# Kernel tuning notes

Measured on AMD Instinct MI355X. Metric: run time of the kernel, lower is better.

The kernel has to match this reference:

```python
import jax, jax.numpy as jnp
import numpy as np

D = 4          # guide-feature dimension (in_channels_feature)
NV = D + 1     # simplex vertices / lattice remainders
BASE = 128     # per-coordinate key encoding base
OFF = 64
SENT = np.int32(2 ** 30)  # sentinel hash for unused slots


def _elevation_matrix(d):
    # Adams et al. elevation: cf = f * scale; elevated = E @ cf, built densely.
    E = np.zeros((d + 1, d), np.float32)
    E[0, :] = 1.0
    for i in range(1, d + 1):
        E[i, i - 1] = -i
        E[i, i:] = 1.0
    scale = 1.0 / np.sqrt((np.arange(d) + 1.0) * (np.arange(d) + 2.0))
    scale = scale * (d + 1.0) * np.sqrt(2.0 / 3.0)  # inv_std_dev
    return (E * scale[None, :]).astype(np.float32)


def _neighbor_offsets(d):
    # lattice axis vectors u_j (first d coords): u_j[i] = d if i==j else -1
    U = -np.ones((d + 1, d), np.int64)
    for j in range(d):
        U[j, j] = d
    offs = []
    for m in range(2 ** (d + 1) - 1):  # all subsets of axes except the full set
        c = [(m >> j) & 1 for j in range(d + 1)]
        offs.append(sum(c[j] * U[j] for j in range(d + 1)))
    return np.stack(offs).astype(np.int32)  # (F, d), F = 2^(d+1)-1


_EMB = jnp.asarray(_elevation_matrix(D))          # (NV, D)
_OFFS = jnp.asarray(_neighbor_offsets(D))         # (F, D)
_POW = jnp.asarray((BASE ** np.arange(D)).astype(np.int32))


def _encode(keys):  # (..., D) int32 -> (...,) int32 perfect hash within range
    k = jnp.clip(keys, -OFF, OFF - 1) + OFF
    return (k * _POW).sum(-1)


def _lattice_filter(feat, dat, Wk):
    # feat: (N, D) guide features; dat: (N, Cin); Wk: (Cout, Cin, F)
    N = feat.shape[0]
    M0 = N * NV  # max distinct lattice points
    elev = feat @ _EMB.T                      # (N, NV)
    g = jnp.round(elev / NV) * NV             # nearest remainder-0 point
    gi = jnp.round(g).astype(jnp.int32)
    s = gi.sum(-1) // NV                      # exact: coords are multiples of NV
    diff = elev - g
    order = jnp.argsort(-diff, axis=-1)       # stable descending sort of residuals
    rank = jnp.argsort(order, axis=-1).astype(jnp.int32) + s[:, None]
    low, high = rank < 0, rank > D
    rank = jnp.where(low, rank + NV, jnp.where(high, rank - NV, rank))
    gi = jnp.where(low, gi + NV, jnp.where(high, gi - NV, gi))
    t = (elev - gi.astype(elev.dtype)) / NV
    rows = jnp.arange(N)[:, None]
    bary = jnp.zeros((N, D + 2), elev.dtype)
    bary = bary.at[rows, D - rank].add(t)
    bary = bary.at[rows, NV - rank].add(1.0 - t)
    bary = bary.at[:, 0].add(1.0 + bary[:, D + 1])
    bary = bary[:, :NV]                       # (N, NV) barycentric weights
    # simplex vertex keys, first D coords only (last is -sum)
    kk = jnp.arange(NV, dtype=jnp.int32)[None, :, None]       # vertex color
    add = jnp.where(rank[:, None, :D] >= NV - kk, kk - NV, kk)
    keys = gi[:, None, :D] + add              # (N, NV, D)
    codes = _encode(keys)                     # (N, NV)
    # --- dedup lattice points (sort + first-occurrence ranks) ---
    flat = codes.reshape(-1)
    sortv = jnp.sort(flat)
    is_new = jnp.concatenate([jnp.ones((1,), bool), sortv[1:] != sortv[:-1]])
    urank = jnp.cumsum(is_new) - 1
    uniq = jnp.full((M0,), SENT, jnp.int32).at[urank].set(sortv)  # sorted uniques
    idx = jnp.searchsorted(uniq, flat)        # (M0,) slot of each (point,vertex)
    # --- splat ---
    Cin = dat.shape[1]
    vals = (dat[:, None, :] * bary[:, :, None]).reshape(M0, Cin)
    table = jnp.zeros((M0, Cin), dat.dtype).at[idx].add(vals)
    ukeys = jnp.zeros((M0, D), jnp.int32).at[idx].set(keys.reshape(M0, D))
    # --- blur: learned conv over lattice neighborhood ---
    ncodes = _encode(ukeys[:, None, :] + _OFFS[None, :, :])   # (M0, F)
    pos = jnp.clip(jnp.searchsorted(uniq, ncodes), 0, M0 - 1)
    valid = (uniq[pos] == ncodes)[..., None]
    gathered = table[pos] * valid             # (M0, F, Cin)
    out_lat = jnp.einsum('mfc,ocf->mo', gathered, Wk)  # (M0, Cout)
    # --- slice ---
    out = jnp.einsum('nk,nko->no', bary, out_lat[idx.reshape(N, NV)])
    return out  # (N, Cout)


def setup_inputs() -> dict:
    key = jax.random.key(0)
    k1, k2, k3, k4 = jax.random.split(key, 4)
    B, Cin, Cout, H, W = 4, 64, 64, 32, 32
    F = 2 ** (D + 1) - 1  # 31 = get_filter_size(1, D)
    return {
        'data': jax.random.normal(k1, (B, Cin, H, W), jnp.float32),
        'features': jax.random.normal(k2, (B, D, H, W), jnp.float32),
        'weights': 0.02 * jax.random.normal(k3, (Cout, Cin, 1, F), jnp.float32),
        'bias': 0.1 * jax.random.normal(k4, (1, 1, 1, Cout), jnp.float32),
        'bias_multiplier': jnp.ones((1, 1, 1, H * W), jnp.float32),
    }


def reference(data, features, weights, bias, bias_multiplier):
    B, Cin, H, W = data.shape
    N = H * W
    feat = features.reshape(B, D, N).transpose(0, 2, 1)   # (B, N, D)
    dat = data.reshape(B, Cin, N).transpose(0, 2, 1)      # (B, N, Cin)
    Wk = weights[:, :, 0, :]                              # (Cout, Cin, F)
    out = jax.vmap(lambda f, x: _lattice_filter(f, x, Wk))(feat, dat)  # (B, N, Cout)
    out = out + bias.reshape(-1)[None, None, :] * bias_multiplier.reshape(-1)[None, :, None]
    Cout = Wk.shape[0]
    return out.transpose(0, 2, 1).reshape(B, Cout, H, W)
```

## Files before the change

### kernel.cpp

```cpp
#include <hip/hip_runtime.h>
#include <hip/hip_bf16.h>
#include <stdint.h>

#define DD 4
#define NVERT 5
#define NPTS 1024
#define BATCH 4
#define M0 5120
#define CIN 64
#define COUT 64
#define NF 31
#define KTOT 1984
#define CAP 16384
#define CAPMASK (CAP-1)
#define SENTV 1073741824
#define ZROW (BATCH*M0)

using bf16x8 = __attribute__((ext_vector_type(8))) short;
using f32x4  = __attribute__((ext_vector_type(4))) float;

__device__ __forceinline__ unsigned short f2bf(float x){
  unsigned int u = __float_as_uint(x);
  u = (u + 0x7FFFu + ((u >> 16) & 1u)) >> 16;
  return (unsigned short)u;
}

__device__ __forceinline__ uint32_t hslot(int code){
  return (((uint32_t)code * 2654435761u) >> 18) & CAPMASK;
}

__device__ __forceinline__ void pv_math(const float* feat, int g, int* code_out, float* bary_out){
  int p = g / NVERT, kk = g % NVERT;
  int b = p >> 10, n = p & 1023;
  const float* fb = feat + (size_t)b * DD * NPTS + n;
  float f0 = fb[0], f1 = fb[NPTS], f2 = fb[2 * NPTS], f3 = fb[3 * NPTS];

  float elev[5];
  elev[0] =  f0 * 2.886751345948129f  + f1 * 1.6666666666666667f + f2 * 1.1785113019775793f + f3 * 0.9128709291752769f;
  elev[1] = -f0 * 2.886751345948129f  + f1 * 1.6666666666666667f + f2 * 1.1785113019775793f + f3 * 0.9128709291752769f;
  elev[2] =  f1 * -3.3333333333333335f + f2 * 1.1785113019775793f + f3 * 0.9128709291752769f;
  elev[3] =  f2 * -3.535533905932738f  + f3 * 0.9128709291752769f;
  elev[4] =  f3 * -3.6514837167011076f;

  int gi[5]; float diff[5]; int sum = 0;
  #pragma unroll
  for (int i = 0; i < 5; i++){
    float gg = rintf(elev[i] * 0.2f) * 5.0f;
    gi[i] = (int)rintf(gg);
    sum += gi[i];
    diff[i] = elev[i] - gg;
  }
  int s = sum / 5;

  int rank[5];
  #pragma unroll
  for (int i = 0; i < 5; i++){
    int r = 0;
    #pragma unroll
    for (int j = 0; j < 5; j++)
      r += (diff[j] > diff[i]) || (diff[j] == diff[i] && j < i);
    rank[i] = r + s;
  }
  #pragma unroll
  for (int i = 0; i < 5; i++){
    if (rank[i] < 0)      { rank[i] += NVERT; gi[i] += NVERT; }
    else if (rank[i] > DD){ rank[i] -= NVERT; gi[i] -= NVERT; }
  }

  float bary[6] = {0.f,0.f,0.f,0.f,0.f,0.f};
  #pragma unroll
  for (int i = 0; i < 5; i++){
    float tt = (elev[i] - (float)gi[i]) * 0.2f;
    bary[DD - rank[i]]    += tt;
    bary[NVERT - rank[i]] += 1.0f - tt;
  }
  bary[0] += 1.0f + bary[5];

  float bk = bary[0];
  #pragma unroll
  for (int i = 1; i < 5; i++) if (i == kk) bk = bary[i];

  int code = 0;
  #pragma unroll
  for (int j = 0; j < DD; j++){
    int add = (rank[j] >= NVERT - kk) ? (kk - NVERT) : kk;
    int key = gi[j] + add;
    key = min(63, max(-64, key));
    code += (key + 64) << (7 * j);
  }
  *code_out = code;
  *bary_out = bk;
}

__global__ void k_a(const float* __restrict__ wk, const float* __restrict__ data,
                    const float* __restrict__ feat,
                    int* __restrict__ hc, int* __restrict__ hu, int* __restrict__ uc,
                    float4* __restrict__ table4, float4* __restrict__ outlat4,
                    unsigned short* __restrict__ bpf, float* __restrict__ dat_t,
                    int* __restrict__ codes_pv, float* __restrict__ bary_pv){
  int bid = blockIdx.x, tid = threadIdx.x;
  if (bid < 64){
    __shared__ float tile[64][65];
    int b = bid >> 4, n0 = (bid & 15) * 64;
    int nl = tid & 63;
    #pragma unroll
    for (int i = 0; i < 16; i++){
      int c = (tid >> 6) * 16 + i;
      tile[c][nl] = data[(((size_t)b * 64 + c) << 10) + n0 + nl];
    }
    __syncthreads();
    #pragma unroll
    for (int i = 0; i < 16; i++){
      int nn = (tid >> 6) * 16 + i;
      dat_t[(((size_t)b << 10) + n0 + nn) * 64 + (tid & 63)] = tile[tid & 63][nn];
    }
  } else if (bid < 144){
    int g = (bid - 64) * 256 + tid;
    int code; float bk;
    pv_math(feat, g, &code, &bk);
    codes_pv[g] = code;
    bary_pv[g]  = bk;
  } else if (bid < 640){
    int e = (bid - 144) * 256 + tid;
    int frag = e >> 9, l = (e >> 3) & 63, j = e & 7;
    int f = frag >> 3, h = (frag >> 2) & 1, g = frag & 3;
    int col = g * 16 + (l & 15);
    int c = h * 32 + ((l >> 4) << 3) + j;
    bpf[e] = f2bf(wk[(col * CIN + c) * NF + f]);
  } else {
    int g = (bid - 640) * 256 + tid;
    int stride = 384 * 256;
    for (int i = g; i < BATCH * CAP; i += stride){ hc[i] = SENTV; hu[i] = -1; }
    if (g < BATCH) uc[g] = 0;
    float4 z = {0.f,0.f,0.f,0.f};
    for (int i = g; i < BATCH * M0 * CIN / 4; i += stride) table4[i] = z;
    for (int i = g; i < BATCH * M0 * COUT / 4; i += stride) outlat4[i] = z;
  }
}

__global__ void k_insert(const int* __restrict__ codes_pv,
                         int* __restrict__ hash_code, int* __restrict__ hash_uid,
                         int* __restrict__ ucount, int* __restrict__ ukeys){
  __shared__ int lhash[512];
  int tid = threadIdx.x;
  lhash[tid] = SENTV; lhash[tid + 256] = SENTV;
  __syncthreads();

  int g = blockIdx.x * 256 + tid;
  int b = g / M0;
  int code = codes_pv[g];

  uint32_t lh = (((uint32_t)code * 2654435761u) >> 21) & 511;
  bool rep = false;
  while (true){
    int prev = atomicCAS(&lhash[lh], SENTV, code);
    if (prev == SENTV){ rep = true; break; }
    if (prev == code) break;
    lh = (lh + 1) & 511;
  }

  int myslot = -1;
  if (rep){
    int* hc = hash_code + b * CAP;
    uint32_t h = hslot(code);
    while (true){
      int prev = atomicCAS(&hc[h], SENTV, code);
      if (prev == SENTV){ myslot = (int)h; break; }
      if (prev == code) break;
      h = (h + 1) & CAPMASK;
    }
  }

  unsigned long long mask = __ballot(myslot >= 0);
  if (mask){
    int lane = tid & 63;
    int cnt = __popcll(mask);
    int leader = __ffsll((unsigned long long)mask) - 1;
    int base = 0;
    if (lane == leader) base = atomicAdd(&ucount[b], cnt);
    base = __shfl(base, leader);
    if (myslot >= 0){
      int rank = __popcll(mask & ((1ull << lane) - 1ull));
      int uid = base + rank;
      hash_uid[b * CAP + myslot] = uid;
      int* uk = ukeys + ((size_t)(b * M0 + uid)) * DD;
      #pragma unroll
      for (int j = 0; j < DD; j++) uk[j] = ((code >> (7 * j)) & 127) - 64;
    }
  }
}

__global__ void k_sn(const float* __restrict__ dat_t, const int* __restrict__ codes_pv,
                     const float* __restrict__ bary_pv, const int* __restrict__ hash_code,
                     const int* __restrict__ hash_uid, const int* __restrict__ ucount,
                     const int* __restrict__ ukeys,
                     int* __restrict__ idx_pv, float* __restrict__ table,
                     int* __restrict__ nuid){
  int bid = blockIdx.x, tid = threadIdx.x;
  if (bid < BATCH * NPTS / 4){
    __shared__ int   us[4][8];
    __shared__ float wbs[4][8];
    int w = tid >> 6, lane = tid & 63;
    int p = bid * 4 + w;
    int b = p >> 10;
    float v = dat_t[((size_t)p << 6) + lane];
    if (lane < NVERT){
      int code = codes_pv[p * NVERT + lane];
      const int* hc = hash_code + b * CAP;
      uint32_t h = hslot(code);
      while (hc[h] != code) h = (h + 1) & CAPMASK;
      int uid = hash_uid[b * CAP + h];
      us[w][lane]  = uid;
      wbs[w][lane] = bary_pv[p * NVERT + lane];
      idx_pv[p * NVERT + lane] = uid;
    }
    __syncthreads();
    int rot = p % NVERT;
    #pragma unroll
    for (int kq = 0; kq < NVERT; kq++){
      int kk = kq + rot; if (kk >= NVERT) kk -= NVERT;
      atomicAdd(&table[(((size_t)(b * M0 + us[w][kk])) << 6) + lane], v * wbs[w][kk]);
    }
  } else {
    int e = (bid - BATCH * NPTS / 4) * 256 + tid;
    int f = e & 31;
    int idx = e >> 5;
    int b = idx / M0, m = idx - b * M0;
    int g = ZROW;
    if (f < NF && m < ucount[b]){
      const int* uk = ukeys + ((size_t)idx) * DD;
      int pc = __popc(f);
      int code = 0;
      #pragma unroll
      for (int j = 0; j < DD; j++){
        int key = uk[j] + 5 * ((f >> j) & 1) - pc;
        key = min(63, max(-64, key));
        code += (key + 64) << (7 * j);
      }
      const int* hc = hash_code + b * CAP;
      uint32_t h = hslot(code);
      while (true){
        int v = hc[h];
        if (v == code){ g = b * M0 + hash_uid[b * CAP + h]; break; }
        if (v == SENTV) break;
        h = (h + 1) & CAPMASK;
      }
    }
    nuid[e] = g;
  }
}

__global__ void k_tobf(const float* __restrict__ table, const int* __restrict__ ucount,
                       unsigned short* __restrict__ table_bf){
  int g = blockIdx.x * blockDim.x + threadIdx.x;
  if (g < 8){
    bf16x8 z = {0,0,0,0,0,0,0,0};
    *(bf16x8*)(table_bf + ((size_t)ZROW << 6) + g * 8) = z;
  }
  int row = g >> 3;
  int b = row / M0;
  if (row - b * M0 >= ucount[b]) return;
  size_t base = (size_t)g * 8;
  const float4* s4 = (const float4*)(table + base);
  float4 x = s4[0], y = s4[1];
  bf16x8 v;
  v[0] = (short)f2bf(x.x); v[1] = (short)f2bf(x.y);
  v[2] = (short)f2bf(x.z); v[3] = (short)f2bf(x.w);
  v[4] = (short)f2bf(y.x); v[5] = (short)f2bf(y.y);
  v[6] = (short)f2bf(y.z); v[7] = (short)f2bf(y.w);
  *(bf16x8*)(table_bf + base) = v;
}

__launch_bounds__(512, 4)
__global__ void k_conv(const int* __restrict__ ucount, const int* __restrict__ nuid,
                       const unsigned short* __restrict__ table_bf,
                       const unsigned short* __restrict__ bpf,
                       float* __restrict__ out_lat){
  __shared__ int gidx_s[64 * 33];
  __shared__ float red[3][2][64][9];

  int blk = blockIdx.x;
  int b    = blk / 160;
  int r    = blk % 160;
  int m0   = (r >> 1) * 64;
  int half = r & 1;
  if (m0 >= ucount[b]) return;

  int tid = threadIdx.x;
  {
    int base = (b * M0 + m0) << 5;
    #pragma unroll
    for (int i = 0; i < 4; i++){
      int idx = tid + i * 512;
      gidx_s[(idx >> 5) * 33 + (idx & 31)] = nuid[base + idx];
    }
  }
  __syncthreads();

  int lane = tid & 63, wave = tid >> 6;
  int wm = wave & 1, wk = wave >> 1;
  int arow = wm * 32 + (lane & 15);
  int acol = (lane >> 4) * 8;
  const unsigned short* bf_lane = bpf + ((size_t)lane << 3);

  f32x4 acc0[4], acc1[4];
  #pragma unroll
  for (int g = 0; g < 4; g++){
    acc0[g] = (f32x4){0.f,0.f,0.f,0.f};
    acc1[g] = (f32x4){0.f,0.f,0.f,0.f};
  }

  const int kfsA[2][5] = {{0,4,8,12,16},{16,20,24,28,31}};
  int f0 = kfsA[half][wk], f1 = kfsA[half][wk + 1], flast = f1 - 1;

  const unsigned short* r0p = table_bf + (((size_t)gidx_s[arow * 33 + f0]) << 6) + acol;
  const unsigned short* r1p = table_bf + (((size_t)gidx_s[(arow + 16) * 33 + f0]) << 6) + acol;
  bf16x8 A00 = *(const bf16x8*)(r0p);
  bf16x8 A01 = *(const bf16x8*)(r0p + 32);
  bf16x8 A10 = *(const bf16x8*)(r1p);
  bf16x8 A11 = *(const bf16x8*)(r1p + 32);

  #pragma unroll 2
  for (int f = f0; f < f1; f++){
    bf16x8 c00 = A00, c01 = A01, c10 = A10, c11 = A11;
    int fn = f + 1 > flast ? flast : f + 1;
    const unsigned short* n0p = table_bf + (((size_t)gidx_s[arow * 33 + fn]) << 6) + acol;
    const unsigned short* n1p = table_bf + (((size_t)gidx_s[(arow + 16) * 33 + fn]) << 6) + acol;
    A00 = *(const bf16x8*)(n0p);
    A01 = *(const bf16x8*)(n0p + 32);
    A10 = *(const bf16x8*)(n1p);
    A11 = *(const bf16x8*)(n1p + 32);

    int fr = f << 3;
    #pragma unroll
    for (int g = 0; g < 4; g++){
      bf16x8 B0 = *(const bf16x8*)(bf_lane + ((size_t)(fr + g)     << 9));
      bf16x8 B1 = *(const bf16x8*)(bf_lane + ((size_t)(fr + 4 + g) << 9));
      acc0[g] = __builtin_amdgcn_mfma_f32_16x16x32_bf16(c00, B0, acc0[g], 0, 0, 0);
      acc0[g] = __builtin_amdgcn_mfma_f32_16x16x32_bf16(c01, B1, acc0[g], 0, 0, 0);
      acc1[g] = __builtin_amdgcn_mfma_f32_16x16x32_bf16(c10, B0, acc1[g], 0, 0, 0);
      acc1[g] = __builtin_amdgcn_mfma_f32_16x16x32_bf16(c11, B1, acc1[g], 0, 0, 0);
    }
  }

  #pragma unroll
  for (int g = 0; g < 4; g++){
    if (wk > 0){
      #pragma unroll
      for (int q = 0; q < 4; q++){
        red[wk - 1][wm][lane][q]     = acc0[g][q];
        red[wk - 1][wm][lane][4 + q] = acc1[g][q];
      }
    }
    __syncthreads();
    if (wk == 0){
      #pragma unroll
      for (int rr = 0; rr < 3; rr++){
        #pragma unroll
        for (int q = 0; q < 4; q++){
          acc0[g][q] += red[rr][wm][lane][q];
          acc1[g][q] += red[rr][wm][lane][4 + q];
        }
      }
    }
    __syncthreads();
  }

  if (wk == 0){
    int q4 = (lane >> 4) * 4, col = lane & 15;
    #pragma unroll
    for (int i = 0; i < 2; i++){
      #pragma unroll
      for (int q = 0; q < 4; q++){
        int m = m0 + wm * 32 + i * 16 + q4 + q;
        float* orow = out_lat + (((size_t)(b * M0 + m)) << 6);
        #pragma unroll
        for (int g = 0; g < 4; g++){
          atomicAdd(&orow[g * 16 + col], (i == 0) ? acc0[g][q] : acc1[g][q]);
        }
      }
    }
  }
}

__global__ void k_slice(const float* __restrict__ bary_pv, const int* __restrict__ idx_pv,
                        const float* __restrict__ out_lat, const float* __restrict__ bias,
                        const float* __restrict__ bmul, float* __restrict__ out){
  __shared__ float tile[16][65];
  int b = blockIdx.x >> 6, n0 = (blockIdx.x & 63) * 16;
  int tid = threadIdx.x;
  int wave = tid >> 6, o = tid & 63;
  float bo = bias[o];
  #pragma unroll
  for (int i = 0; i < 4; i++){
    int n = wave * 4 + i;
    int p = (b << 10) + n0 + n;
    float acc = bo * bmul[n0 + n];
    int base = p * NVERT;
    #pragma unroll
    for (int kk = 0; kk < NVERT; kk++){
      int u = idx_pv[base + kk];
      acc += bary_pv[base + kk] * out_lat[(((size_t)(b * M0 + u)) << 6) + o];
    }
    tile[n][o] = acc;
  }
  __syncthreads();
  int nl = tid & 15;
  #pragma unroll
  for (int i = 0; i < 4; i++){
    int o2 = (tid >> 4) + i * 16;
    out[(((size_t)b * 64 + o2) << 10) + n0 + nl] = tile[nl][o2];
  }
}

extern "C" void kernel_launch(void* const* d_in, const int* in_sizes, int n_in,
                              void* d_out, int out_size, void* d_ws, size_t ws_size,
                              hipStream_t stream){
  const float* data = (const float*)d_in[0];
  const float* feat = (const float*)d_in[1];
  const float* wk   = (const float*)d_in[2];
  const float* bias = (const float*)d_in[3];
  const float* bmul = (const float*)d_in[4];
  float* out = (float*)d_out;

  char* ws = (char*)d_ws;
  size_t off = 0;
  auto alloc = [&](size_t bytes){
    void* p = ws + off;
    off = (off + bytes + 255) & ~(size_t)255;
    return p;
  };
  int*   codes_pv = (int*)  alloc((size_t)BATCH * M0 * 4);
  float* bary_pv  = (float*)alloc((size_t)BATCH * M0 * 4);
  int*   idx_pv   = (int*)  alloc((size_t)BATCH * M0 * 4);
  int*   hash_code= (int*)  alloc((size_t)BATCH * CAP * 4);
  int*   hash_uid = (int*)  alloc((size_t)BATCH * CAP * 4);
  int*   ucount   = (int*)  alloc(256);
  int*   ukeys    = (int*)  alloc((size_t)BATCH * M0 * DD * 4);
  float* table    = (float*)alloc((size_t)BATCH * M0 * CIN * 4);
  float* out_lat  = (float*)alloc((size_t)BATCH * M0 * COUT * 4);
  unsigned short* bpf      = (unsigned short*)alloc((size_t)COUT * KTOT * 2);
  unsigned short* table_bf = (unsigned short*)alloc(((size_t)BATCH * M0 + 8) * CIN * 2);
  float* dat_t    = (float*)alloc((size_t)BATCH * NPTS * CIN * 4);
  int*   nuid     = (int*)  alloc((size_t)BATCH * M0 * 32 * 4);

  k_a     <<<1024, 256, 0, stream>>>(wk, data, feat, hash_code, hash_uid, ucount,
                                     (float4*)table, (float4*)out_lat, bpf, dat_t,
                                     codes_pv, bary_pv);
  k_insert<<<BATCH * M0 / 256, 256, 0, stream>>>(codes_pv, hash_code, hash_uid, ucount, ukeys);
  k_sn    <<<BATCH * NPTS / 4 + BATCH * M0 * 32 / 256, 256, 0, stream>>>(
            dat_t, codes_pv, bary_pv, hash_code, hash_uid, ucount, ukeys,
            idx_pv, table, nuid);
  k_tobf  <<<BATCH * M0 * CIN / 8 / 256, 256, 0, stream>>>(table, ucount, table_bf);
  k_conv  <<<BATCH * 160, 512, 0, stream>>>(ucount, nuid, table_bf, bpf, out_lat);
  k_slice <<<BATCH * 64, 256, 0, stream>>>(bary_pv, idx_pv, out_lat, bias, bmul, out);
}
```

Before: 43.04 us.

## Repartition conv work so each wave covers all 64 rows over two filter taps

The k_conv block now has each of its 8 waves handle all 64 lattice rows for two filter offsets, instead of a 2x4 split of rows and offset ranges. Each B-fragment load from the weight tensor is reused across four row groups rather than two, which cuts redundant weight traffic per MFMA. The cost is a larger cross-wave reduction through shared memory (7 waves, 16 floats per lane, 4 rounds with barriers), more accumulator registers (64 floats), and losing the software prefetch of the next A rows.

```diff
diff --git a/kernel.cpp b/kernel.cpp
--- a/kernel.cpp
+++ b/kernel.cpp
@@ -277,7 +277,7 @@
                        const unsigned short* __restrict__ bpf,
                        float* __restrict__ out_lat){
   __shared__ int gidx_s[64 * 33];
-  __shared__ float red[3][2][64][9];
+  __shared__ float red[7][64][17];
 
   int blk = blockIdx.x;
   int b    = blk / 160;
@@ -298,85 +298,81 @@
   __syncthreads();
 
   int lane = tid & 63, wave = tid >> 6;
-  int wm = wave & 1, wk = wave >> 1;
-  int arow = wm * 32 + (lane & 15);
+  int rl = lane & 15;
   int acol = (lane >> 4) * 8;
   const unsigned short* bf_lane = bpf + ((size_t)lane << 3);
 
-  f32x4 acc0[4], acc1[4];
-  #pragma unroll
-  for (int g = 0; g < 4; g++){
-    acc0[g] = (f32x4){0.f,0.f,0.f,0.f};
-    acc1[g] = (f32x4){0.f,0.f,0.f,0.f};
-  }
-
-  const int kfsA[2][5] = {{0,4,8,12,16},{16,20,24,28,31}};
-  int f0 = kfsA[half][wk], f1 = kfsA[half][wk + 1], flast = f1 - 1;
-
-  const unsigned short* r0p = table_bf + (((size_t)gidx_s[arow * 33 + f0]) << 6) + acol;
-  const unsigned short* r1p = table_bf + (((size_t)gidx_s[(arow + 16) * 33 + f0]) << 6) + acol;
-  bf16x8 A00 = *(const bf16x8*)(r0p);
-  bf16x8 A01 = *(const bf16x8*)(r0p + 32);
-  bf16x8 A10 = *(const bf16x8*)(r1p);
-  bf16x8 A11 = *(const bf16x8*)(r1p + 32);
-
-  #pragma unroll 2
+  f32x4 acc[4][4];
+  #pragma unroll
+  for (int rg = 0; rg < 4; rg++)
+    #pragma unroll
+    for (int g = 0; g < 4; g++)
+      acc[rg][g] = (f32x4){0.f,0.f,0.f,0.f};
+
+  int f0 = half * 16 + wave * 2;
+  int f1 = f0 + 2; if (f1 > NF) f1 = NF;
+
   for (int f = f0; f < f1; f++){
-    bf16x8 c00 = A00, c01 = A01, c10 = A10, c11 = A11;
-    int fn = f + 1 > flast ? flast : f + 1;
-    const unsigned short* n0p = table_bf + (((size_t)gidx_s[arow * 33 + fn]) << 6) + acol;
-    const unsigned short* n1p = table_bf + (((size_t)gidx_s[(arow + 16) * 33 + fn]) << 6) + acol;
-    A00 = *(const bf16x8*)(n0p);
-    A01 = *(const bf16x8*)(n0p + 32);
-    A10 = *(const bf16x8*)(n1p);
-    A11 = *(const bf16x8*)(n1p + 32);
-
+    bf16x8 A0_0, A0_1, A1_0, A1_1, A2_0, A2_1, A3_0, A3_1;
+    {
+      const unsigned short* p0 = table_bf + (((size_t)gidx_s[(rl     ) * 33 + f]) << 6) + acol;
+      const unsigned short* p1 = table_bf + (((size_t)gidx_s[(rl + 16) * 33 + f]) << 6) + acol;
+      const unsigned short* p2 = table_bf + (((size_t)gidx_s[(rl + 32) * 33 + f]) << 6) + acol;
+      const unsigned short* p3 = table_bf + (((size_t)gidx_s[(rl + 48) * 33 + f]) << 6) + acol;
+      A0_0 = *(const bf16x8*)(p0); A0_1 = *(const bf16x8*)(p0 + 32);
+      A1_0 = *(const bf16x8*)(p1); A1_1 = *(const bf16x8*)(p1 + 32);
+      A2_0 = *(const bf16x8*)(p2); A2_1 = *(const bf16x8*)(p2 + 32);
+      A3_0 = *(const bf16x8*)(p3); A3_1 = *(const bf16x8*)(p3 + 32);
+    }
     int fr = f << 3;
     #pragma unroll
     for (int g = 0; g < 4; g++){
       bf16x8 B0 = *(const bf16x8*)(bf_lane + ((size_t)(fr + g)     << 9));
       bf16x8 B1 = *(const bf16x8*)(bf_lane + ((size_t)(fr + 4 + g) << 9));
-      acc0[g] = __builtin_amdgcn_mfma_f32_16x16x32_bf16(c00, B0, acc0[g], 0, 0, 0);
-      acc0[g] = __builtin_amdgcn_mfma_f32_16x16x32_bf16(c01, B1, acc0[g], 0, 0, 0);
-      acc1[g] = __builtin_amdgcn_mfma_f32_16x16x32_bf16(c10, B0, acc1[g], 0, 0, 0);
-      acc1[g] = __builtin_amdgcn_mfma_f32_16x16x32_bf16(c11, B1, acc1[g], 0, 0, 0);
-    }
-  }
-
-  #pragma unroll
-  for (int g = 0; g < 4; g++){
-    if (wk > 0){
+      acc[0][g] = __builtin_amdgcn_mfma_f32_16x16x32_bf16(A0_0, B0, acc[0][g], 0, 0, 0);
+      acc[0][g] = __builtin_amdgcn_mfma_f32_16x16x32_bf16(A0_1, B1, acc[0][g], 0, 0, 0);
+      acc[1][g] = __builtin_amdgcn_mfma_f32_16x16x32_bf16(A1_0, B0, acc[1][g], 0, 0, 0);
+      acc[1][g] = __builtin_amdgcn_mfma_f32_16x16x32_bf16(A1_1, B1, acc[1][g], 0, 0, 0);
+      acc[2][g] = __builtin_amdgcn_mfma_f32_16x16x32_bf16(A2_0, B0, acc[2][g], 0, 0, 0);
+      acc[2][g] = __builtin_amdgcn_mfma_f32_16x16x32_bf16(A2_1, B1, acc[2][g], 0, 0, 0);
+      acc[3][g] = __builtin_amdgcn_mfma_f32_16x16x32_bf16(A3_0, B0, acc[3][g], 0, 0, 0);
+      acc[3][g] = __builtin_amdgcn_mfma_f32_16x16x32_bf16(A3_1, B1, acc[3][g], 0, 0, 0);
+    }
+  }
+
+  #pragma unroll
+  for (int rg = 0; rg < 4; rg++){
+    if (wave > 0){
+      #pragma unroll
+      for (int g = 0; g < 4; g++)
+        #pragma unroll
+        for (int q = 0; q < 4; q++)
+          red[wave - 1][lane][g * 4 + q] = acc[rg][g][q];
+    }
+    __syncthreads();
+    if (wave == 0){
+      #pragma unroll
+      for (int w = 0; w < 7; w++)
+        #pragma unroll
+        for (int g = 0; g < 4; g++)
+          #pragma unroll
+          for (int q = 0; q < 4; q++)
+            acc[rg][g][q] += red[w][lane][g * 4 + q];
+    }
+    __syncthreads();
+  }
+
+  if (wave == 0){
+    int q4 = (lane >> 4) * 4, col = lane & 15;
+    #pragma unroll
+    for (int rg = 0; rg < 4; rg++){
       #pragma unroll
       for (int q = 0; q < 4; q++){
-        red[wk - 1][wm][lane][q]     = acc0[g][q];
-        red[wk - 1][wm][lane][4 + q] = acc1[g][q];
-      }
-    }
-    __syncthreads();
-    if (wk == 0){
-      #pragma unroll
-      for (int rr = 0; rr < 3; rr++){
-        #pragma unroll
-        for (int q = 0; q < 4; q++){
-          acc0[g][q] += red[rr][wm][lane][q];
-          acc1[g][q] += red[rr][wm][lane][4 + q];
-        }
-      }
-    }
-    __syncthreads();
-  }
-
-  if (wk == 0){
-    int q4 = (lane >> 4) * 4, col = lane & 15;
-    #pragma unroll
-    for (int i = 0; i < 2; i++){
-      #pragma unroll
-      for (int q = 0; q < 4; q++){
-        int m = m0 + wm * 32 + i * 16 + q4 + q;
+        int m = m0 + rg * 16 + q4 + q;
         float* orow = out_lat + (((size_t)(b * M0 + m)) << 6);
         #pragma unroll
         for (int g = 0; g < 4; g++){
-          atomicAdd(&orow[g * 16 + col], (i == 0) ? acc0[g][q] : acc1[g][q]);
+          atomicAdd(&orow[g * 16 + col], acc[rg][g][q]);
         }
       }
     }
```

After: 41.86 us, median of 2. -2.7%, faster.
